# Performance work log

Hardware: AMD Instinct MI355X
Metric: run time of the kernel (lower is better)

Reference implementation:

```python
import jax, jax.numpy as jnp
import numpy as np

RMS_EPS = 1e-5
L2_EPS = 1e-8


def _rms_norm(x, eps=RMS_EPS):
    return x * jax.lax.rsqrt(jnp.mean(x * x, axis=-1, keepdims=True) + eps)


def _l2_norm(x, eps=L2_EPS):
    return jnp.linalg.norm(x, ord=2, axis=-1, keepdims=True) + eps


def setup_inputs() -> dict:
    key = jax.random.key(0)
    kq, kk, kv = jax.random.split(key, 3)
    B, H, S, D = 4, 16, 4096, 64
    Q = jax.random.normal(kq, (B, H, S, D), dtype=jnp.float32)
    K = jax.random.normal(kk, (B, H, S, D), dtype=jnp.float32)
    V = jax.random.normal(kv, (B, H, S, D), dtype=jnp.float32)
    return {"Q": Q, "K": K, "V": V}


def reference(Q, K, V):
    # v_swiglu = SiLU(V) * V
    v_swiglu = jax.nn.silu(V) * V
    # causal cumulative sum over sequence dim
    c = jnp.cumsum(v_swiglu, axis=-2)
    c_n = _rms_norm(c)
    # gating scalar per (b,h,s): ||Q|| + ||K|| + 1
    r = _l2_norm(Q) + _l2_norm(K) + 1.0
    mstate = c_n / r
    # SwiGLU combine: V + SiLU(mstate) * V, then final RMSNorm
    out0 = V + jax.nn.silu(mstate) * V
    return _rms_norm(out0)
```

## Files before the change

kernel.cpp:

```cpp
#include <hip/hip_runtime.h>
#include <math.h>

#define BH 64
#define SEQ 4096
#define DIM 64
#define CHUNK 32
#define NCHUNK (SEQ / CHUNK)
#define NCH_TOT (BH * NCHUNK)
#define P1_WPB 4
#define CPB 8
#define SBLOCKS (NCH_TOT / CPB)

__device__ __forceinline__ float fast_rcp(float x)  { return __builtin_amdgcn_rcpf(x); }
__device__ __forceinline__ float fast_rsqrt(float x){ return __builtin_amdgcn_rsqf(x); }
__device__ __forceinline__ float fast_sigmoid(float x) {
    return fast_rcp(1.0f + __expf(-x));
}

__device__ __forceinline__ float red16(float x) {
    x += __shfl_xor(x, 1);
    x += __shfl_xor(x, 2);
    x += __shfl_xor(x, 4);
    x += __shfl_xor(x, 8);
    return x;
}

__global__ __launch_bounds__(256) void k_partials(const float* __restrict__ V,
                                                  float* __restrict__ P) {
    const int wave = threadIdx.x >> 6;
    const int lane = threadIdx.x & 63;
    const int g = lane >> 4, h = lane & 15;
    const int chunk = blockIdx.x * P1_WPB + wave;

    const float4* v4 = (const float4*)(V + (size_t)chunk * (CHUNK * DIM));
    float a0 = 0.f, a1 = 0.f, a2 = 0.f, a3 = 0.f;
#pragma unroll
    for (int j0 = 0; j0 < CHUNK; j0 += 4) {
        float4 v = v4[(j0 + g) * 16 + h];
        a0 += v.x * v.x * fast_sigmoid(v.x);
        a1 += v.y * v.y * fast_sigmoid(v.y);
        a2 += v.z * v.z * fast_sigmoid(v.z);
        a3 += v.w * v.w * fast_sigmoid(v.w);
    }
#pragma unroll
    for (int m = 16; m < 64; m <<= 1) {
        a0 += __shfl_xor(a0, m);
        a1 += __shfl_xor(a1, m);
        a2 += __shfl_xor(a2, m);
        a3 += __shfl_xor(a3, m);
    }
    if (g == 0) {
        float4 o = {a0, a1, a2, a3};
        ((float4*)(P + (size_t)chunk * DIM))[h] = o;
    }
}

__device__ __forceinline__ void scan_step(const float4* __restrict__ q4,
                                          const float4* __restrict__ k4,
                                          const float4* __restrict__ v4,
                                          float4* __restrict__ o4,
                                          float (&cb)[4],
                                          int idx, int g,
                                          int up16, int up32, int src3) {
    float4 v = v4[idx];
    float4 q = q4[idx];
    float4 k = k4[idx];

    float q2 = red16(q.x*q.x + q.y*q.y + q.z*q.z + q.w*q.w);
    float k2 = red16(k.x*k.x + k.y*k.y + k.z*k.z + k.w*k.w);
    float r  = sqrtf(q2) + sqrtf(k2) + 1.0f;

    float s0 = v.x * v.x * fast_sigmoid(v.x);
    float s1 = v.y * v.y * fast_sigmoid(v.y);
    float s2v = v.z * v.z * fast_sigmoid(v.z);
    float s3 = v.w * v.w * fast_sigmoid(v.w);

    float t0 = __shfl(s0, up16); s0 += (g >= 1) ? t0 : 0.f;
    float t1 = __shfl(s1, up16); s1 += (g >= 1) ? t1 : 0.f;
    float t2 = __shfl(s2v, up16); s2v += (g >= 1) ? t2 : 0.f;
    float t3 = __shfl(s3, up16); s3 += (g >= 1) ? t3 : 0.f;

    float u0 = __shfl(s0, up32); s0 += (g >= 2) ? u0 : 0.f;
    float u1 = __shfl(s1, up32); s1 += (g >= 2) ? u1 : 0.f;
    float u2 = __shfl(s2v, up32); s2v += (g >= 2) ? u2 : 0.f;
    float u3 = __shfl(s3, up32); s3 += (g >= 2) ? u3 : 0.f;

    float w0 = __shfl(s0, src3);
    float w1 = __shfl(s1, src3);
    float w2 = __shfl(s2v, src3);
    float w3 = __shfl(s3, src3);

    float c0 = cb[0] + s0;  cb[0] += w0;
    float c1 = cb[1] + s1;  cb[1] += w1;
    float c2 = cb[2] + s2v; cb[2] += w2;
    float c3 = cb[3] + s3;  cb[3] += w3;

    float cs = red16(c0*c0 + c1*c1 + c2*c2 + c3*c3);
    float rms_c = fast_rsqrt(cs * (1.0f / 64.0f) + 1e-5f);
    float s = rms_c * fast_rcp(r);

    float m0 = c0 * s; float o0 = v.x * (1.0f + m0 * fast_sigmoid(m0));
    float m1 = c1 * s; float o1 = v.y * (1.0f + m1 * fast_sigmoid(m1));
    float m2 = c2 * s; float o2 = v.z * (1.0f + m2 * fast_sigmoid(m2));
    float m3 = c3 * s; float o3 = v.w * (1.0f + m3 * fast_sigmoid(m3));

    float os = red16(o0*o0 + o1*o1 + o2*o2 + o3*o3);
    float rms_o = fast_rsqrt(os * (1.0f / 64.0f) + 1e-5f);
    float4 outv = {o0 * rms_o, o1 * rms_o, o2 * rms_o, o3 * rms_o};
    o4[idx] = outv;
}

__global__ __launch_bounds__(256, 4) void k_scan(const float* __restrict__ Q,
                                                 const float* __restrict__ K,
                                                 const float* __restrict__ V,
                                                 const float* __restrict__ P,
                                                 float* __restrict__ O) {
    __shared__ float segsum[4][DIM];
    __shared__ float excl[CPB][DIM];

    const int t    = threadIdx.x;
    const int lane = t & 63;
    const int wave = t >> 6;
    const int b    = blockIdx.x;
    const int bib  = b & 15;
    const float* pslab = P + (size_t)(b >> 4) * (NCHUNK * DIM);

    float run = 0.f, run8 = 0.f, run16 = 0.f, run24 = 0.f;
#pragma unroll
    for (int j = 0; j < 32; ++j) {
        if (j == 8)  run8  = run;
        if (j == 16) run16 = run;
        if (j == 24) run24 = run;
        run += pslab[(wave * 32 + j) * DIM + lane];
    }
    segsum[wave][lane] = run;
    __syncthreads();

    const int seg_t = bib >> 2;
    const int off   = (bib & 3) * 8;
    if (wave == seg_t) {
        float carry = 0.f;
#pragma unroll
        for (int s = 0; s < 4; ++s)
            if (s < seg_t) carry += segsum[s][lane];
        float ws = carry + (off == 0 ? 0.f :
                            off == 8 ? run8 :
                            off == 16 ? run16 : run24);
#pragma unroll
        for (int i = 0; i < CPB; ++i) {
            excl[i][lane] = ws;
            ws += pslab[(seg_t * 32 + off + i) * DIM + lane];
        }
    }
    __syncthreads();

    const int g = lane >> 4, h = lane & 15;
    const int cA = b * CPB + 2 * wave;
    const int cB = cA + 1;
    const size_t baseA = (size_t)cA * (CHUNK * DIM);
    const size_t baseB = (size_t)cB * (CHUNK * DIM);
    const float4* qA = (const float4*)(Q + baseA);
    const float4* kA = (const float4*)(K + baseA);
    const float4* vA = (const float4*)(V + baseA);
    float4*       oA = (float4*)(O + baseA);
    const float4* qB = (const float4*)(Q + baseB);
    const float4* kB = (const float4*)(K + baseB);
    const float4* vB = (const float4*)(V + baseB);
    float4*       oB = (float4*)(O + baseB);

    float4 ea = ((const float4*)excl[2 * wave])[h];
    float4 eb = ((const float4*)excl[2 * wave + 1])[h];
    float cbA[4] = {ea.x, ea.y, ea.z, ea.w};
    float cbB[4] = {eb.x, eb.y, eb.z, eb.w};

    const int up16 = (lane + 48) & 63;
    const int up32 = (lane + 32) & 63;
    const int src3 = 48 + h;

#pragma unroll
    for (int j0 = 0; j0 < CHUNK; j0 += 4) {
        const int idx = (j0 + g) * 16 + h;
        scan_step(qA, kA, vA, oA, cbA, idx, g, up16, up32, src3);
        scan_step(qB, kB, vB, oB, cbB, idx, g, up16, up32, src3);
    }
}

extern "C" void kernel_launch(void* const* d_in, const int* in_sizes, int n_in,
                              void* d_out, int out_size, void* d_ws, size_t ws_size,
                              hipStream_t stream) {
    const float* Q = (const float*)d_in[0];
    const float* K = (const float*)d_in[1];
    const float* V = (const float*)d_in[2];
    float* O = (float*)d_out;
    float* P = (float*)d_ws;

    k_partials<<<NCH_TOT / P1_WPB, 256, 0, stream>>>(V, P);
    k_scan<<<SBLOCKS, 256, 0, stream>>>(Q, K, V, P, O);
}
```

Measured before the change: 225.1 us.

## Fuse partials and scan into one kernel with decoupled look-back prefix

Replaces the two-kernel scheme (chunk partial sums, then a block-level scan that rereads partials) with a single kernel. Blocks take ordered IDs from an atomic ticket, compute the chunk sums of SwiGLU(V), and publish aggregate and inclusive prefixes through status flags using a decoupled look-back. Each block then runs the original per-chunk scan. This removes one kernel launch and the partials round trip, at the cost of adding a memset, spin-waiting on predecessors, and serial dependency chains across blocks.

```diff
diff --git a/kernel.cpp b/kernel.cpp
--- a/kernel.cpp
+++ b/kernel.cpp
@@ -7,15 +7,17 @@
 #define CHUNK 32
 #define NCHUNK (SEQ / CHUNK)
 #define NCH_TOT (BH * NCHUNK)
-#define P1_WPB 4
 #define CPB 8
-#define SBLOCKS (NCH_TOT / CPB)
+#define NBLK (NCH_TOT / CPB)
+#define BPB (NCHUNK / CPB)
+#define TPB 256
 
 __device__ __forceinline__ float fast_rcp(float x)  { return __builtin_amdgcn_rcpf(x); }
 __device__ __forceinline__ float fast_rsqrt(float x){ return __builtin_amdgcn_rsqf(x); }
 __device__ __forceinline__ float fast_sigmoid(float x) {
     return fast_rcp(1.0f + __expf(-x));
 }
+__device__ __forceinline__ float swiglu(float v) { return v * v * fast_sigmoid(v); }
 
 __device__ __forceinline__ float red16(float x) {
     x += __shfl_xor(x, 1);
@@ -23,36 +25,6 @@
     x += __shfl_xor(x, 4);
     x += __shfl_xor(x, 8);
     return x;
-}
-
-__global__ __launch_bounds__(256) void k_partials(const float* __restrict__ V,
-                                                  float* __restrict__ P) {
-    const int wave = threadIdx.x >> 6;
-    const int lane = threadIdx.x & 63;
-    const int g = lane >> 4, h = lane & 15;
-    const int chunk = blockIdx.x * P1_WPB + wave;
-
-    const float4* v4 = (const float4*)(V + (size_t)chunk * (CHUNK * DIM));
-    float a0 = 0.f, a1 = 0.f, a2 = 0.f, a3 = 0.f;
-#pragma unroll
-    for (int j0 = 0; j0 < CHUNK; j0 += 4) {
-        float4 v = v4[(j0 + g) * 16 + h];
-        a0 += v.x * v.x * fast_sigmoid(v.x);
-        a1 += v.y * v.y * fast_sigmoid(v.y);
-        a2 += v.z * v.z * fast_sigmoid(v.z);
-        a3 += v.w * v.w * fast_sigmoid(v.w);
-    }
-#pragma unroll
-    for (int m = 16; m < 64; m <<= 1) {
-        a0 += __shfl_xor(a0, m);
-        a1 += __shfl_xor(a1, m);
-        a2 += __shfl_xor(a2, m);
-        a3 += __shfl_xor(a3, m);
-    }
-    if (g == 0) {
-        float4 o = {a0, a1, a2, a3};
-        ((float4*)(P + (size_t)chunk * DIM))[h] = o;
-    }
 }
 
 __device__ __forceinline__ void scan_step(const float4* __restrict__ q4,
@@ -70,10 +42,10 @@
     float k2 = red16(k.x*k.x + k.y*k.y + k.z*k.z + k.w*k.w);
     float r  = sqrtf(q2) + sqrtf(k2) + 1.0f;
 
-    float s0 = v.x * v.x * fast_sigmoid(v.x);
-    float s1 = v.y * v.y * fast_sigmoid(v.y);
-    float s2v = v.z * v.z * fast_sigmoid(v.z);
-    float s3 = v.w * v.w * fast_sigmoid(v.w);
+    float s0 = swiglu(v.x);
+    float s1 = swiglu(v.y);
+    float s2v = swiglu(v.z);
+    float s3 = swiglu(v.w);
 
     float t0 = __shfl(s0, up16); s0 += (g >= 1) ? t0 : 0.f;
     float t1 = __shfl(s1, up16); s1 += (g >= 1) ? t1 : 0.f;
@@ -110,68 +82,108 @@
     o4[idx] = outv;
 }
 
-__global__ __launch_bounds__(256, 4) void k_scan(const float* __restrict__ Q,
-                                                 const float* __restrict__ K,
-                                                 const float* __restrict__ V,
-                                                 const float* __restrict__ P,
-                                                 float* __restrict__ O) {
-    __shared__ float segsum[4][DIM];
-    __shared__ float excl[CPB][DIM];
-
-    const int t    = threadIdx.x;
-    const int lane = t & 63;
-    const int wave = t >> 6;
-    const int b    = blockIdx.x;
-    const int bib  = b & 15;
-    const float* pslab = P + (size_t)(b >> 4) * (NCHUNK * DIM);
-
-    float run = 0.f, run8 = 0.f, run16 = 0.f, run24 = 0.f;
-#pragma unroll
-    for (int j = 0; j < 32; ++j) {
-        if (j == 8)  run8  = run;
-        if (j == 16) run16 = run;
-        if (j == 24) run24 = run;
-        run += pslab[(wave * 32 + j) * DIM + lane];
-    }
-    segsum[wave][lane] = run;
+__global__ __launch_bounds__(TPB, 4) void k_fused_lb(const float* __restrict__ Q,
+                                                     const float* __restrict__ K,
+                                                     const float* __restrict__ V,
+                                                     float* __restrict__ O,
+                                                     int* __restrict__ ticket,
+                                                     int* __restrict__ status,
+                                                     float* __restrict__ agg,
+                                                     float* __restrict__ inc) {
+    __shared__ int vbid_s;
+    __shared__ float cagg[CPB][DIM];
+    __shared__ float bexcl[DIM];
+
+    if (threadIdx.x == 0) vbid_s = atomicAdd(ticket, 1);
     __syncthreads();
-
-    const int seg_t = bib >> 2;
-    const int off   = (bib & 3) * 8;
-    if (wave == seg_t) {
-        float carry = 0.f;
-#pragma unroll
-        for (int s = 0; s < 4; ++s)
-            if (s < seg_t) carry += segsum[s][lane];
-        float ws = carry + (off == 0 ? 0.f :
-                            off == 8 ? run8 :
-                            off == 16 ? run16 : run24);
-#pragma unroll
-        for (int i = 0; i < CPB; ++i) {
-            excl[i][lane] = ws;
-            ws += pslab[(seg_t * 32 + off + i) * DIM + lane];
+    const int b    = vbid_s;
+    const int bib  = b & (BPB - 1);
+    const int wave = threadIdx.x >> 6;
+    const int lane = threadIdx.x & 63;
+    const int g = lane >> 4, h = lane & 15;
+
+    const int cA = b * CPB + 2 * wave;
+    const size_t baseA = (size_t)cA * (CHUNK * DIM);
+    const size_t baseB = baseA + (CHUNK * DIM);
+    const float4* vA4 = (const float4*)(V + baseA);
+    const float4* vB4 = (const float4*)(V + baseB);
+
+    float aA0=0.f,aA1=0.f,aA2=0.f,aA3=0.f, aB0=0.f,aB1=0.f,aB2=0.f,aB3=0.f;
+#pragma unroll
+    for (int j0 = 0; j0 < CHUNK; j0 += 4) {
+        const int idx = (j0 + g) * 16 + h;
+        float4 va = vA4[idx];
+        float4 vb = vB4[idx];
+        aA0 += swiglu(va.x); aA1 += swiglu(va.y);
+        aA2 += swiglu(va.z); aA3 += swiglu(va.w);
+        aB0 += swiglu(vb.x); aB1 += swiglu(vb.y);
+        aB2 += swiglu(vb.z); aB3 += swiglu(vb.w);
+    }
+#pragma unroll
+    for (int m = 16; m < 64; m <<= 1) {
+        aA0 += __shfl_xor(aA0, m); aA1 += __shfl_xor(aA1, m);
+        aA2 += __shfl_xor(aA2, m); aA3 += __shfl_xor(aA3, m);
+        aB0 += __shfl_xor(aB0, m); aB1 += __shfl_xor(aB1, m);
+        aB2 += __shfl_xor(aB2, m); aB3 += __shfl_xor(aB3, m);
+    }
+    if (g == 0) {
+        float4 sa = {aA0, aA1, aA2, aA3};
+        float4 sb = {aB0, aB1, aB2, aB3};
+        ((float4*)cagg[2 * wave])[h]     = sa;
+        ((float4*)cagg[2 * wave + 1])[h] = sb;
+    }
+    __syncthreads();
+
+    if (wave == 0) {
+        float bagg = 0.f;
+#pragma unroll
+        for (int i = 0; i < CPB; ++i) bagg += cagg[i][lane];
+        agg[(size_t)b * DIM + lane] = bagg;
+        if (bib == 0) {
+            inc[(size_t)b * DIM + lane] = bagg;
+            __threadfence();
+            if (lane == 0) atomicExch(&status[b], 2);
+            bexcl[lane] = 0.f;
+        } else {
+            __threadfence();
+            if (lane == 0) atomicExch(&status[b], 1);
+            float ex = 0.f;
+            int j = b - 1;
+            for (;;) {
+                int st = 0;
+                if (lane == 0) {
+                    while ((st = atomicAdd(&status[j], 0)) == 0)
+                        __builtin_amdgcn_s_sleep(1);
+                }
+                st = __shfl(st, 0);
+                __threadfence();
+                if (st == 2) { ex += inc[(size_t)j * DIM + lane]; break; }
+                ex += agg[(size_t)j * DIM + lane];
+                --j;
+            }
+            inc[(size_t)b * DIM + lane] = ex + bagg;
+            __threadfence();
+            if (lane == 0) atomicExch(&status[b], 2);
+            bexcl[lane] = ex;
         }
     }
     __syncthreads();
 
-    const int g = lane >> 4, h = lane & 15;
-    const int cA = b * CPB + 2 * wave;
-    const int cB = cA + 1;
-    const size_t baseA = (size_t)cA * (CHUNK * DIM);
-    const size_t baseB = (size_t)cB * (CHUNK * DIM);
-    const float4* qA = (const float4*)(Q + baseA);
-    const float4* kA = (const float4*)(K + baseA);
-    const float4* vA = (const float4*)(V + baseA);
-    float4*       oA = (float4*)(O + baseA);
-    const float4* qB = (const float4*)(Q + baseB);
-    const float4* kB = (const float4*)(K + baseB);
-    const float4* vB = (const float4*)(V + baseB);
-    float4*       oB = (float4*)(O + baseB);
-
-    float4 ea = ((const float4*)excl[2 * wave])[h];
-    float4 eb = ((const float4*)excl[2 * wave + 1])[h];
-    float cbA[4] = {ea.x, ea.y, ea.z, ea.w};
-    float cbB[4] = {eb.x, eb.y, eb.z, eb.w};
+    float4 e0 = ((const float4*)bexcl)[h];
+    float cbA[4] = {e0.x, e0.y, e0.z, e0.w};
+    for (int i = 0; i < 2 * wave; ++i) {
+        float4 t = ((const float4*)cagg[i])[h];
+        cbA[0] += t.x; cbA[1] += t.y; cbA[2] += t.z; cbA[3] += t.w;
+    }
+    float4 tA = ((const float4*)cagg[2 * wave])[h];
+    float cbB[4] = {cbA[0] + tA.x, cbA[1] + tA.y, cbA[2] + tA.z, cbA[3] + tA.w};
+
+    const float4* qA4 = (const float4*)(Q + baseA);
+    const float4* kA4 = (const float4*)(K + baseA);
+    float4*       oA4 = (float4*)(O + baseA);
+    const float4* qB4 = (const float4*)(Q + baseB);
+    const float4* kB4 = (const float4*)(K + baseB);
+    float4*       oB4 = (float4*)(O + baseB);
 
     const int up16 = (lane + 48) & 63;
     const int up32 = (lane + 32) & 63;
@@ -180,8 +192,8 @@
 #pragma unroll
     for (int j0 = 0; j0 < CHUNK; j0 += 4) {
         const int idx = (j0 + g) * 16 + h;
-        scan_step(qA, kA, vA, oA, cbA, idx, g, up16, up32, src3);
-        scan_step(qB, kB, vB, oB, cbB, idx, g, up16, up32, src3);
+        scan_step(qA4, kA4, vA4, oA4, cbA, idx, g, up16, up32, src3);
+        scan_step(qB4, kB4, vB4, oB4, cbB, idx, g, up16, up32, src3);
     }
 }
 
@@ -192,8 +204,12 @@
     const float* K = (const float*)d_in[1];
     const float* V = (const float*)d_in[2];
     float* O = (float*)d_out;
-    float* P = (float*)d_ws;
-
-    k_partials<<<NCH_TOT / P1_WPB, 256, 0, stream>>>(V, P);
-    k_scan<<<SBLOCKS, 256, 0, stream>>>(Q, K, V, P, O);
-}
+
+    int*   status = (int*)d_ws;
+    int*   ticket = status + NBLK;
+    float* agg    = (float*)((char*)d_ws + 8192);
+    float* inc    = agg + (size_t)NBLK * DIM;
+
+    hipMemsetAsync(d_ws, 0, 8192, stream);
+    k_fused_lb<<<NBLK, TPB, 0, stream>>>(Q, K, V, O, ticket, status, agg, inc);
+}
```

Result: slower. 488.9 us (+117.1%).
